# Optimization experiments

Hardware: AMD Instinct MI355X
Metric: run time of the kernel (lower is better)

Reference implementation:

```python
import jax, jax.numpy as jnp
import numpy as np

N, G, E, F, H = 100000, 32768, 1000000, 128, 128

def _mlp(x, w1, b1, w2, b2):
    # Linear -> SiLU -> Linear
    return jax.nn.silu(x @ w1 + b1) @ w2 + b2

def setup_inputs() -> dict:
    key = jax.random.key(0)
    ks = jax.random.split(key, 24)
    s = 0.02
    p = lambda k, shp: (jax.random.normal(k, shp, dtype=jnp.float32) * s)
    inp = {
        "node_features": jax.random.normal(ks[0], (N, F), dtype=jnp.float32),
        "node_pos": jax.random.normal(ks[1], (N, 3), dtype=jnp.float32),
        "grid_pos": jax.random.normal(ks[2], (G, 3), dtype=jnp.float32),
        "edge_index": jax.random.randint(ks[3], (2, E), 0, G, dtype=jnp.int64),
        "orientations": jax.random.normal(ks[4], (N, 3, 3), dtype=jnp.float32),
        # node_model
        "nw1": p(ks[5], (F, H)), "nb1": p(ks[6], (H,)),
        "nw2": p(ks[7], (H, H)), "nb2": p(ks[8], (H,)),
        # edge_model
        "ew1": p(ks[9], (6, H)), "eb1": p(ks[10], (H,)),
        "ew2": p(ks[11], (H, H)), "eb2": p(ks[12], (H,)),
        # message_model
        "mw1": p(ks[13], (2 * H, H)), "mb1": p(ks[14], (H,)),
        "mw2": p(ks[15], (H, H)), "mb2": p(ks[16], (H,)),
        # update_model
        "uw1": p(ks[17], (H, H)), "ub1": p(ks[18], (H,)),
        "uw2": p(ks[19], (H, H)), "ub2": p(ks[20], (H,)),
    }
    return inp

def reference(node_features, node_pos, grid_pos, edge_index, orientations,
              nw1, nb1, nw2, nb2, ew1, eb1, ew2, eb2,
              mw1, mb1, mw2, mb2, uw1, ub1, uw2, ub2):
    src, tgt = edge_index[0], edge_index[1]
    # node MLP on all points [N, H]
    node_h = _mlp(node_features, nw1, nb1, nw2, nb2)
    # per-edge geometry
    pos_src = node_pos[src]                     # [E, 3]
    rel_pos = grid_pos[tgt] - pos_src           # [E, 3]
    # bmm(rel_pos[e,1,3], orientations[src][e,3,3]) -> [E, 3]
    rot = jnp.einsum("ej,ejk->ek", rel_pos, orientations[src])
    edge_attr = jnp.concatenate([pos_src, rot], axis=-1)       # [E, 6]
    edge_h = _mlp(edge_attr, ew1, eb1, ew2, eb2)               # [E, H]
    msg_in = jnp.concatenate([node_h[src], edge_h], axis=-1)   # [E, 2H]
    msg = _mlp(msg_in, mw1, mb1, mw2, mb2)                     # [E, H]
    # scatter-mean to grid
    num_grid = grid_pos.shape[0]
    sums = jax.ops.segment_sum(msg, tgt, num_segments=num_grid)             # [G, H]
    counts = jax.ops.segment_sum(jnp.ones((msg.shape[0],), msg.dtype), tgt,
                                 num_segments=num_grid)
    grid_feat = sums / jnp.clip(counts, 1.0)[:, None]
    return _mlp(grid_feat, uw1, ub1, uw2, ub2)
```

## Files before the change

### kernel.cpp

```cpp
#include <hip/hip_runtime.h>

#define P 136

typedef __attribute__((ext_vector_type(8))) short short8;
typedef __attribute__((ext_vector_type(4))) float f32x4;

__device__ __forceinline__ unsigned short f2bf(float f) {
  union { float f; unsigned u; } v; v.f = f;
  unsigned u = v.u + 0x7fffu + ((v.u >> 16) & 1u);
  return (unsigned short)(u >> 16);
}
__device__ __forceinline__ float bf2f(unsigned short h) {
  union { unsigned u; float f; } v; v.u = ((unsigned)h) << 16;
  return v.f;
}
__device__ __forceinline__ unsigned pack2bf(float x, float y) {
  union { float f; unsigned u; } a, b; a.f = x; b.f = y;
  return __builtin_amdgcn_perm(b.u + 0x8000u, a.u + 0x8000u, 0x07060302u);
}
__device__ __forceinline__ float silu_f(float x) {
  float e = __expf(-x);
  return x * __builtin_amdgcn_rcpf(1.0f + e);
}

__device__ __forceinline__ void load_A128(const unsigned short* __restrict__ W,
                                          int m0w, int l16, int q, short8 a[2][4]) {
#pragma unroll
  for (int rt = 0; rt < 2; ++rt)
#pragma unroll
    for (int kt = 0; kt < 4; ++kt)
      a[rt][kt] = *(const short8*)&W[(m0w + rt * 16 + l16) * 128 + kt * 32 + q * 8];
}

__device__ __forceinline__ void gemm_T(const short8 a[2][4],
                                       const unsigned short* sB,
                                       int l16, int q, f32x4 acc[2][8]) {
#pragma unroll
  for (int kt = 0; kt < 4; ++kt)
#pragma unroll
    for (int ct = 0; ct < 8; ++ct) {
      short8 b = *(const short8*)&sB[(ct * 16 + l16) * P + kt * 32 + q * 8];
      acc[0][ct] = __builtin_amdgcn_mfma_f32_16x16x32_bf16(a[0][kt], b, acc[0][ct], 0, 0, 0);
      acc[1][ct] = __builtin_amdgcn_mfma_f32_16x16x32_bf16(a[1][kt], b, acc[1][ct], 0, 0, 0);
    }
}

template <bool SILU>
__device__ __forceinline__ void epilogue_T(const f32x4 acc[2][8], const float* bias,
                                           unsigned short* sOut, int m0w, int l16,
                                           int q) {
#pragma unroll
  for (int rt = 0; rt < 2; ++rt) {
    int f0 = m0w + rt * 16 + q * 4;
    float4 bv = *(const float4*)&bias[f0];
#pragma unroll
    for (int ct = 0; ct < 8; ++ct) {
      float v0 = acc[rt][ct][0] + bv.x, v1 = acc[rt][ct][1] + bv.y;
      float v2 = acc[rt][ct][2] + bv.z, v3 = acc[rt][ct][3] + bv.w;
      if (SILU) { v0 = silu_f(v0); v1 = silu_f(v1); v2 = silu_f(v2); v3 = silu_f(v3); }
      uint2 w; w.x = pack2bf(v0, v1); w.y = pack2bf(v2, v3);
      *(uint2*)&sOut[(ct * 16 + l16) * P + f0] = w;
    }
  }
}

__global__ __launch_bounds__(256) void fold_hist_kernel(
    const float* __restrict__ nw1, const float* __restrict__ nw2,
    const float* __restrict__ nb2, const float* __restrict__ ew2,
    const float* __restrict__ eb2, const float* __restrict__ mw1,
    const float* __restrict__ mb1, const float* __restrict__ mw2,
    const float* __restrict__ uw1, const float* __restrict__ uw2,
    const float* __restrict__ ew1,
    unsigned short* __restrict__ nw1t, unsigned short* __restrict__ wnt,
    unsigned short* __restrict__ wct, unsigned short* __restrict__ mw2t,
    unsigned short* __restrict__ uw1t, unsigned short* __restrict__ uw2t,
    unsigned short* __restrict__ ew1t8,
    float* __restrict__ bn, float* __restrict__ bc,
    const int* __restrict__ eidx, int* __restrict__ hist, int E) {
  if (blockIdx.x >= 64) {
    int e = (blockIdx.x - 64) * 256 + threadIdx.x;
    if (e < E) atomicAdd(&hist[eidx[E + e]], 1);
    return;
  }
  int b = blockIdx.x * 2 + (threadIdx.x >> 7);
  int t = threadIdx.x & 127;
  float accn = 0.f, accc = 0.f;
  for (int j = 0; j < 128; ++j) {
    accn += nw2[t * 128 + j] * mw1[j * 128 + b];
    accc += ew2[t * 128 + j] * mw1[(128 + j) * 128 + b];
  }
  wnt[b * 128 + t] = f2bf(accn);
  wct[b * 128 + t] = f2bf(accc);
  nw1t[b * 128 + t] = f2bf(nw1[t * 128 + b]);
  mw2t[b * 128 + t] = f2bf(mw2[t * 128 + b]);
  uw1t[b * 128 + t] = f2bf(uw1[t * 128 + b]);
  uw2t[b * 128 + t] = f2bf(uw2[t * 128 + b]);
  if (t < 8) ew1t8[b * 8 + t] = (t < 6) ? f2bf(ew1[t * 128 + b]) : (unsigned short)0;
  if (b == 0) {
    float sn = 0.f, sc = 0.f;
    for (int j = 0; j < 128; ++j) {
      sn += nb2[j] * mw1[j * 128 + t];
      sc += eb2[j] * mw1[(128 + j) * 128 + t];
    }
    bn[t] = sn;
    bc[t] = mb1[t] + sc;
  }
}

__global__ __launch_bounds__(1024) void scan_kernel(const int* __restrict__ hist,
                                                    int* __restrict__ cursor, int G) {
  __shared__ int s[1024];
  int tid = threadIdx.x;
  int per = (G + 1023) >> 10;
  int b0 = tid * per;
  int sum = 0;
  for (int i = 0; i < per; ++i)
    if (b0 + i < G) sum += hist[b0 + i];
  s[tid] = sum;
  __syncthreads();
  for (int off = 1; off < 1024; off <<= 1) {
    int v = (tid >= off) ? s[tid - off] : 0;
    __syncthreads();
    s[tid] += v;
    __syncthreads();
  }
  int run = s[tid] - sum;
  for (int i = 0; i < per; ++i)
    if (b0 + i < G) {
      cursor[b0 + i] = run;
      run += hist[b0 + i];
    }
}

__global__ __launch_bounds__(256, 3) void scatter_node_kernel(
    const int* __restrict__ eidx, int* __restrict__ cursor,
    int2* __restrict__ st, int E, int nScat,
    const float* __restrict__ x, const float* __restrict__ nb1,
    const unsigned short* __restrict__ nw1t, const unsigned short* __restrict__ wnt,
    const float* __restrict__ bn, unsigned short* __restrict__ node_pre, int N) {
  __shared__ __align__(16) unsigned short s_x[128 * P];
  __shared__ __align__(16) float s_b1[128];
  __shared__ __align__(16) float s_bn[128];

  if (blockIdx.x < (unsigned)nScat) {
    int e = blockIdx.x * 256 + threadIdx.x;
    if (e < E) {
      int tg = eidx[E + e];
      int pos = atomicAdd(&cursor[tg], 1);
      st[pos] = make_int2(eidx[e], tg);
    }
    return;
  }

  int tid = threadIdx.x;
  long base = (long)(blockIdx.x - nScat) * 128;

#pragma unroll
  for (int i = 0; i < 16; ++i) {
    int flat = tid + i * 256;
    int row = flat >> 5;
    int c4 = (flat & 31) << 2;
    float4 v = make_float4(0.f, 0.f, 0.f, 0.f);
    if (base + row < N) v = *(const float4*)&x[(base + row) * 128 + c4];
    uint2 w; w.x = pack2bf(v.x, v.y); w.y = pack2bf(v.z, v.w);
    *(uint2*)&s_x[row * P + c4] = w;
  }
  if (tid < 128) { s_b1[tid] = nb1[tid]; s_bn[tid] = bn[tid]; }
  __syncthreads();

  int wave = tid >> 6, lane = tid & 63;
  int q = lane >> 4, l16 = lane & 15;
  int m0w = wave * 32;

  short8 a1[2][4];
  load_A128(nw1t, m0w, l16, q, a1);
  f32x4 acc[2][8];
#pragma unroll
  for (int rt = 0; rt < 2; ++rt)
#pragma unroll
    for (int ct = 0; ct < 8; ++ct) acc[rt][ct] = (f32x4){0.f, 0.f, 0.f, 0.f};
  gemm_T(a1, s_x, l16, q, acc);
  __syncthreads();
  epilogue_T<true>(acc, s_b1, s_x, m0w, l16, q);
  __syncthreads();

  short8 a2[2][4];
  load_A128(wnt, m0w, l16, q, a2);
#pragma unroll
  for (int rt = 0; rt < 2; ++rt)
#pragma unroll
    for (int ct = 0; ct < 8; ++ct) acc[rt][ct] = (f32x4){0.f, 0.f, 0.f, 0.f};
  gemm_T(a2, s_x, l16, q, acc);

#pragma unroll
  for (int rt = 0; rt < 2; ++rt) {
    int f0 = m0w + rt * 16 + q * 4;
    float4 bv = *(const float4*)&s_bn[f0];
#pragma unroll
    for (int ct = 0; ct < 8; ++ct) {
      long n = base + ct * 16 + l16;
      if (n < N) {
        uint2 w;
        w.x = pack2bf(acc[rt][ct][0] + bv.x, acc[rt][ct][1] + bv.y);
        w.y = pack2bf(acc[rt][ct][2] + bv.z, acc[rt][ct][3] + bv.w);
        *(uint2*)&node_pre[n * 128 + f0] = w;
      }
    }
  }
}

__global__ __launch_bounds__(256, 3) void edge_kernel(
    const int2* __restrict__ st_sorted, const float* __restrict__ node_pos,
    const float* __restrict__ grid_pos, const float* __restrict__ ori,
    const unsigned short* __restrict__ ew1t8, const float* __restrict__ eb1,
    const unsigned short* __restrict__ wct, const float* __restrict__ bc,
    const unsigned short* __restrict__ node_pre, float* __restrict__ sums, int E) {
  __shared__ __align__(16) unsigned short s_h[128 * P];
  __shared__ int s_src[128];
  __shared__ int s_tgt[128];
  __shared__ __align__(16) float s_eb1[128];
  __shared__ __align__(16) float s_bc[128];

  int tid = threadIdx.x;
  int base = blockIdx.x * 128;

  if (tid < 128) {
    s_eb1[tid] = eb1[tid];
    s_bc[tid] = bc[tid];
    int eg = base + tid;
    int s = 0, tg = -1;
    float a0 = 0.f, a1 = 0.f, a2 = 0.f, a3 = 0.f, a4 = 0.f, a5 = 0.f;
    if (eg < E) {
      int2 st = st_sorted[eg];
      s = st.x; tg = st.y;
      float2 p01 = *(const float2*)&node_pos[s * 3];
      float pz = node_pos[s * 3 + 2];
      float2 g01 = *(const float2*)&grid_pos[tg * 3];
      float gz = grid_pos[tg * 3 + 2];
      float4 o0 = *(const float4*)&ori[(long)s * 9];
      float4 o1 = *(const float4*)&ori[(long)s * 9 + 4];
      float o8 = ori[(long)s * 9 + 8];
      float rx = g01.x - p01.x, ry = g01.y - p01.y, rz = gz - pz;
      a0 = p01.x; a1 = p01.y; a2 = pz;
      a3 = rx * o0.x + ry * o0.w + rz * o1.z;
      a4 = rx * o0.y + ry * o1.x + rz * o1.w;
      a5 = rx * o0.z + ry * o1.y + rz * o8;
    }
    s_src[tid] = s;
    s_tgt[tid] = tg;
    uint4 w0;
    w0.x = pack2bf(a0, a1); w0.y = pack2bf(a2, a3); w0.z = pack2bf(a4, a5); w0.w = 0u;
    *(uint4*)&s_h[tid * P] = w0;
  }

  int wave = tid >> 6, lane = tid & 63;
  int q = lane >> 4, l16 = lane & 15;
  int m0w = wave * 32;
  short8 z8 = (short8){0, 0, 0, 0, 0, 0, 0, 0};

  short8 ae0 = z8, ae1 = z8;
  if (q == 0) {
    ae0 = *(const short8*)&ew1t8[(m0w + l16) * 8];
    ae1 = *(const short8*)&ew1t8[(m0w + 16 + l16) * 8];
  }

  __syncthreads();

  short8 pre[8];
#pragma unroll
  for (int ct = 0; ct < 8; ++ct) {
    long srow = (long)s_src[ct * 16 + l16] * 128;
    pre[ct] = *(const short8*)&node_pre[srow + m0w + q * 8];
  }

  f32x4 acc0[2][8];
#pragma unroll
  for (int rt = 0; rt < 2; ++rt)
#pragma unroll
    for (int ct = 0; ct < 8; ++ct) acc0[rt][ct] = (f32x4){0.f, 0.f, 0.f, 0.f};
#pragma unroll
  for (int ct = 0; ct < 8; ++ct) {
    short8 b = z8;
    if (q == 0) b = *(const short8*)&s_h[(ct * 16 + l16) * P];
    acc0[0][ct] = __builtin_amdgcn_mfma_f32_16x16x32_bf16(ae0, b, acc0[0][ct], 0, 0, 0);
    acc0[1][ct] = __builtin_amdgcn_mfma_f32_16x16x32_bf16(ae1, b, acc0[1][ct], 0, 0, 0);
  }
  __syncthreads();

  epilogue_T<true>(acc0, s_eb1, s_h, m0w, l16, q);

  short8 awc[2][4];
  load_A128(wct, m0w, l16, q, awc);

  __syncthreads();

  short8 aI_lo, aI_hi;
#pragma unroll
  for (int j = 0; j < 8; ++j) {
    aI_lo[j] = ((q * 8 + j) == l16) ? (short)0x3F80 : (short)0;
    aI_hi[j] = ((q * 8 + j) == (l16 + 16)) ? (short)0x3F80 : (short)0;
  }
  f32x4 acc[2][8];
#pragma unroll
  for (int ct = 0; ct < 8; ++ct) {
    acc[0][ct] = __builtin_amdgcn_mfma_f32_16x16x32_bf16(
        aI_lo, pre[ct], (f32x4){0.f, 0.f, 0.f, 0.f}, 0, 0, 0);
    acc[1][ct] = __builtin_amdgcn_mfma_f32_16x16x32_bf16(
        aI_hi, pre[ct], (f32x4){0.f, 0.f, 0.f, 0.f}, 0, 0, 0);
  }

  gemm_T(awc, s_h, l16, q, acc);
  __syncthreads();

  epilogue_T<true>(acc, s_bc, s_h, m0w, l16, q);
  __syncthreads();

  {
    int cp = tid & 63;
    int chunk = tid >> 6;
    int c0 = cp * 2;
    int row0 = chunk * 32;
    float v0 = 0.f, v1 = 0.f;
    int cur = s_tgt[row0];
    for (int r = 0; r < 32; ++r) {
      int row = row0 + r;
      int tg = s_tgt[row];
      if (tg != cur) {
        if (cur >= 0) {
          atomicAdd(&sums[(long)cur * 128 + c0], v0);
          atomicAdd(&sums[(long)cur * 128 + c0 + 1], v1);
        }
        v0 = 0.f; v1 = 0.f; cur = tg;
      }
      unsigned w = *(const unsigned*)&s_h[row * P + c0];
      v0 += bf2f((unsigned short)w);
      v1 += bf2f((unsigned short)(w >> 16));
    }
    if (cur >= 0) {
      atomicAdd(&sums[(long)cur * 128 + c0], v0);
      atomicAdd(&sums[(long)cur * 128 + c0 + 1], v1);
    }
  }
}

__global__ __launch_bounds__(256, 3) void grid_kernel(
    const float* __restrict__ sums, const int* __restrict__ hist,
    const float* __restrict__ mb2, const float* __restrict__ ub1,
    const float* __restrict__ ub2, const unsigned short* __restrict__ mw2t,
    const unsigned short* __restrict__ uw1t, const unsigned short* __restrict__ uw2t,
    float* __restrict__ out, int G) {
  __shared__ __align__(16) unsigned short s_x[128 * P];
  __shared__ __align__(16) float s_bm[128];
  __shared__ __align__(16) float s_b1[128];
  __shared__ __align__(16) float s_b2[128];
  int tid = threadIdx.x;
  long base = (long)blockIdx.x * 128;

#pragma unroll
  for (int i = 0; i < 16; ++i) {
    int flat = tid + i * 256;
    int row = flat >> 5;
    int c4 = (flat & 31) << 2;
    float4 v = make_float4(0.f, 0.f, 0.f, 0.f);
    float inv = 1.f;
    if (base + row < G) {
      v = *(const float4*)&sums[(base + row) * 128 + c4];
      int c = hist[base + row];
      inv = __builtin_amdgcn_rcpf((float)(c < 1 ? 1 : c));
    }
    uint2 w; w.x = pack2bf(v.x * inv, v.y * inv); w.y = pack2bf(v.z * inv, v.w * inv);
    *(uint2*)&s_x[row * P + c4] = w;
  }
  if (tid < 128) { s_bm[tid] = mb2[tid]; s_b1[tid] = ub1[tid]; s_b2[tid] = ub2[tid]; }
  __syncthreads();

  int wave = tid >> 6, lane = tid & 63;
  int q = lane >> 4, l16 = lane & 15;
  int m0w = wave * 32;

  f32x4 acc[2][8];
  short8 aw[2][4];

  load_A128(mw2t, m0w, l16, q, aw);
#pragma unroll
  for (int rt = 0; rt < 2; ++rt)
#pragma unroll
    for (int ct = 0; ct < 8; ++ct) acc[rt][ct] = (f32x4){0.f, 0.f, 0.f, 0.f};
  gemm_T(aw, s_x, l16, q, acc);
  __syncthreads();
  epilogue_T<false>(acc, s_bm, s_x, m0w, l16, q);
  __syncthreads();

  load_A128(uw1t, m0w, l16, q, aw);
#pragma unroll
  for (int rt = 0; rt < 2; ++rt)
#pragma unroll
    for (int ct = 0; ct < 8; ++ct) acc[rt][ct] = (f32x4){0.f, 0.f, 0.f, 0.f};
  gemm_T(aw, s_x, l16, q, acc);
  __syncthreads();
  epilogue_T<true>(acc, s_b1, s_x, m0w, l16, q);
  __syncthreads();

  load_A128(uw2t, m0w, l16, q, aw);
#pragma unroll
  for (int rt = 0; rt < 2; ++rt)
#pragma unroll
    for (int ct = 0; ct < 8; ++ct) acc[rt][ct] = (f32x4){0.f, 0.f, 0.f, 0.f};
  gemm_T(aw, s_x, l16, q, acc);

#pragma unroll
  for (int rt = 0; rt < 2; ++rt) {
    int f0 = m0w + rt * 16 + q * 4;
    float4 bv = *(const float4*)&s_b2[f0];
#pragma unroll
    for (int ct = 0; ct < 8; ++ct) {
      long g = base + ct * 16 + l16;
      if (g < G) {
        float4 o = make_float4(acc[rt][ct][0] + bv.x, acc[rt][ct][1] + bv.y,
                               acc[rt][ct][2] + bv.z, acc[rt][ct][3] + bv.w);
        *(float4*)&out[g * 128 + f0] = o;
      }
    }
  }
}

extern "C" void kernel_launch(void* const* d_in, const int* in_sizes, int n_in,
                              void* d_out, int out_size, void* d_ws, size_t ws_size,
                              hipStream_t stream) {
  const float* x    = (const float*)d_in[0];
  const float* npos = (const float*)d_in[1];
  const float* gpos = (const float*)d_in[2];
  const int*   eidx = (const int*)d_in[3];
  const float* ori  = (const float*)d_in[4];
  const float* nw1 = (const float*)d_in[5];
  const float* nb1 = (const float*)d_in[6];
  const float* nw2 = (const float*)d_in[7];
  const float* nb2 = (const float*)d_in[8];
  const float* ew1 = (const float*)d_in[9];
  const float* eb1 = (const float*)d_in[10];
  const float* ew2 = (const float*)d_in[11];
  const float* eb2 = (const float*)d_in[12];
  const float* mw1 = (const float*)d_in[13];
  const float* mb1 = (const float*)d_in[14];
  const float* mw2 = (const float*)d_in[15];
  const float* mb2 = (const float*)d_in[16];
  const float* uw1 = (const float*)d_in[17];
  const float* ub1 = (const float*)d_in[18];
  const float* uw2 = (const float*)d_in[19];
  const float* ub2 = (const float*)d_in[20];

  int N = in_sizes[0] / 128;
  int G = in_sizes[2] / 3;
  int E = in_sizes[3] / 2;

  char* ws = (char*)d_ws;
  size_t off = 0;
  float* sums = (float*)(ws + off);            off += (size_t)G * 128 * 4;
  int* hist = (int*)(ws + off);                off += (size_t)G * 4;
  int* cursor = (int*)(ws + off);              off += (size_t)G * 4;
  unsigned short* node_pre = (unsigned short*)(ws + off); off += (size_t)N * 128 * 2;
  off = (off + 255) & ~(size_t)255;
  unsigned short* w_nw1t = (unsigned short*)(ws + off); off += 128 * 128 * 2;
  unsigned short* w_wnt  = (unsigned short*)(ws + off); off += 128 * 128 * 2;
  unsigned short* w_wct  = (unsigned short*)(ws + off); off += 128 * 128 * 2;
  unsigned short* w_mw2t = (unsigned short*)(ws + off); off += 128 * 128 * 2;
  unsigned short* w_uw1t = (unsigned short*)(ws + off); off += 128 * 128 * 2;
  unsigned short* w_uw2t = (unsigned short*)(ws + off); off += 128 * 128 * 2;
  unsigned short* w_ew1t8 = (unsigned short*)(ws + off); off += 128 * 8 * 2;
  float* bn = (float*)(ws + off); off += 128 * 4;
  float* bc = (float*)(ws + off); off += 128 * 4;

  int2* st_sorted = (int2*)d_out;

  int nScat = (E + 255) / 256;
  int nNode = (N + 127) / 128;
  int nHist = (E + 255) / 256;

  hipMemsetAsync(sums, 0, ((size_t)G * 128 + G) * 4, stream);

  fold_hist_kernel<<<64 + nHist, 256, 0, stream>>>(
      nw1, nw2, nb2, ew2, eb2, mw1, mb1, mw2, uw1, uw2, ew1,
      w_nw1t, w_wnt, w_wct, w_mw2t, w_uw1t, w_uw2t, w_ew1t8, bn, bc,
      eidx, hist, E);
  scan_kernel<<<1, 1024, 0, stream>>>(hist, cursor, G);
  scatter_node_kernel<<<nScat + nNode, 256, 0, stream>>>(
      eidx, cursor, st_sorted, E, nScat,
      x, nb1, w_nw1t, w_wnt, bn, node_pre, N);
  edge_kernel<<<(E + 127) / 128, 256, 0, stream>>>(st_sorted, npos, gpos, ori,
                                                   w_ew1t8, eb1, w_wct, bc,
                                                   node_pre, sums, E);
  grid_kernel<<<(G + 127) / 128, 256, 0, stream>>>(sums, hist, mb2, ub1, ub2,
                                                   w_mw2t, w_uw1t, w_uw2t,
                                                   (float*)d_out, G);
}
```

Baseline: 469.3 us.

## Batch eight edges per thread in hist/scatter, shrink grid tiles, templatize GEMM

The histogram and scatter phases now handle eight edges per thread using int4 loads, which cuts the number of blocks launched. The scan kernel reads and writes counts with int4 where alignment allows. The grid kernel tile drops from 128 to 32 grid points per block, giving four times as many smaller blocks with less shared memory each, which should help occupancy and load balance. The GEMM helper is templated on the column-tile count and seeds the first MFMA with zero instead of clearing accumulators in a separate loop, and the scatter blocks are moved after the node blocks. The trade-off is that smaller grid tiles reload the weights more often, and batching edges leaves fewer threads in flight to hide atomic latency.

```diff
diff --git a/kernel.cpp b/kernel.cpp
--- a/kernel.cpp
+++ b/kernel.cpp
@@ -32,21 +32,25 @@
       a[rt][kt] = *(const short8*)&W[(m0w + rt * 16 + l16) * 128 + kt * 32 + q * 8];
 }
 
+template <int CT, bool INIT>
 __device__ __forceinline__ void gemm_T(const short8 a[2][4],
                                        const unsigned short* sB,
-                                       int l16, int q, f32x4 acc[2][8]) {
+                                       int l16, int q, f32x4 acc[2][CT]) {
+  const f32x4 Z = (f32x4){0.f, 0.f, 0.f, 0.f};
 #pragma unroll
   for (int kt = 0; kt < 4; ++kt)
 #pragma unroll
-    for (int ct = 0; ct < 8; ++ct) {
+    for (int ct = 0; ct < CT; ++ct) {
       short8 b = *(const short8*)&sB[(ct * 16 + l16) * P + kt * 32 + q * 8];
-      acc[0][ct] = __builtin_amdgcn_mfma_f32_16x16x32_bf16(a[0][kt], b, acc[0][ct], 0, 0, 0);
-      acc[1][ct] = __builtin_amdgcn_mfma_f32_16x16x32_bf16(a[1][kt], b, acc[1][ct], 0, 0, 0);
-    }
-}
-
-template <bool SILU>
-__device__ __forceinline__ void epilogue_T(const f32x4 acc[2][8], const float* bias,
+      f32x4 c0 = (INIT && kt == 0) ? Z : acc[0][ct];
+      f32x4 c1 = (INIT && kt == 0) ? Z : acc[1][ct];
+      acc[0][ct] = __builtin_amdgcn_mfma_f32_16x16x32_bf16(a[0][kt], b, c0, 0, 0, 0);
+      acc[1][ct] = __builtin_amdgcn_mfma_f32_16x16x32_bf16(a[1][kt], b, c1, 0, 0, 0);
+    }
+}
+
+template <bool SILU, int CT>
+__device__ __forceinline__ void epilogue_T(const f32x4 acc[2][CT], const float* bias,
                                            unsigned short* sOut, int m0w, int l16,
                                            int q) {
 #pragma unroll
@@ -54,7 +58,7 @@
     int f0 = m0w + rt * 16 + q * 4;
     float4 bv = *(const float4*)&bias[f0];
 #pragma unroll
-    for (int ct = 0; ct < 8; ++ct) {
+    for (int ct = 0; ct < CT; ++ct) {
       float v0 = acc[rt][ct][0] + bv.x, v1 = acc[rt][ct][1] + bv.y;
       float v2 = acc[rt][ct][2] + bv.z, v3 = acc[rt][ct][3] + bv.w;
       if (SILU) { v0 = silu_f(v0); v1 = silu_f(v1); v2 = silu_f(v2); v3 = silu_f(v3); }
@@ -78,8 +82,21 @@
     float* __restrict__ bn, float* __restrict__ bc,
     const int* __restrict__ eidx, int* __restrict__ hist, int E) {
   if (blockIdx.x >= 64) {
-    int e = (blockIdx.x - 64) * 256 + threadIdx.x;
-    if (e < E) atomicAdd(&hist[eidx[E + e]], 1);
+    int e0 = (blockIdx.x - 64) * 2048 + threadIdx.x * 8;
+    if (e0 + 7 < E && (E & 3) == 0) {
+      int4 t0 = *(const int4*)&eidx[E + e0];
+      int4 t1 = *(const int4*)&eidx[E + e0 + 4];
+      atomicAdd(&hist[t0.x], 1); atomicAdd(&hist[t0.y], 1);
+      atomicAdd(&hist[t0.z], 1); atomicAdd(&hist[t0.w], 1);
+      atomicAdd(&hist[t1.x], 1); atomicAdd(&hist[t1.y], 1);
+      atomicAdd(&hist[t1.z], 1); atomicAdd(&hist[t1.w], 1);
+    } else {
+#pragma unroll
+      for (int k = 0; k < 8; ++k) {
+        int e = e0 + k;
+        if (e < E) atomicAdd(&hist[eidx[E + e]], 1);
+      }
+    }
     return;
   }
   int b = blockIdx.x * 2 + (threadIdx.x >> 7);
@@ -113,9 +130,17 @@
   int tid = threadIdx.x;
   int per = (G + 1023) >> 10;
   int b0 = tid * per;
+  bool vec = ((per & 3) == 0) && ((G & 3) == 0) && (b0 + per <= G);
   int sum = 0;
-  for (int i = 0; i < per; ++i)
-    if (b0 + i < G) sum += hist[b0 + i];
+  if (vec) {
+    for (int i = 0; i < per; i += 4) {
+      int4 h = *(const int4*)&hist[b0 + i];
+      sum += h.x + h.y + h.z + h.w;
+    }
+  } else {
+    for (int i = 0; i < per; ++i)
+      if (b0 + i < G) sum += hist[b0 + i];
+  }
   s[tid] = sum;
   __syncthreads();
   for (int off = 1; off < 1024; off <<= 1) {
@@ -125,16 +150,29 @@
     __syncthreads();
   }
   int run = s[tid] - sum;
-  for (int i = 0; i < per; ++i)
-    if (b0 + i < G) {
-      cursor[b0 + i] = run;
-      run += hist[b0 + i];
-    }
+  if (vec) {
+    for (int i = 0; i < per; i += 4) {
+      int4 h = *(const int4*)&hist[b0 + i];
+      int4 c;
+      c.x = run;
+      c.y = c.x + h.x;
+      c.z = c.y + h.y;
+      c.w = c.z + h.z;
+      *(int4*)&cursor[b0 + i] = c;
+      run = c.w + h.w;
+    }
+  } else {
+    for (int i = 0; i < per; ++i)
+      if (b0 + i < G) {
+        cursor[b0 + i] = run;
+        run += hist[b0 + i];
+      }
+  }
 }
 
 __global__ __launch_bounds__(256, 3) void scatter_node_kernel(
     const int* __restrict__ eidx, int* __restrict__ cursor,
-    int2* __restrict__ st, int E, int nScat,
+    int2* __restrict__ st, int E, int nNode,
     const float* __restrict__ x, const float* __restrict__ nb1,
     const unsigned short* __restrict__ nw1t, const unsigned short* __restrict__ wnt,
     const float* __restrict__ bn, unsigned short* __restrict__ node_pre, int N) {
@@ -142,18 +180,45 @@
   __shared__ __align__(16) float s_b1[128];
   __shared__ __align__(16) float s_bn[128];
 
-  if (blockIdx.x < (unsigned)nScat) {
-    int e = blockIdx.x * 256 + threadIdx.x;
-    if (e < E) {
-      int tg = eidx[E + e];
-      int pos = atomicAdd(&cursor[tg], 1);
-      st[pos] = make_int2(eidx[e], tg);
+  if (blockIdx.x >= (unsigned)nNode) {
+    int e0 = (blockIdx.x - nNode) * 2048 + threadIdx.x * 8;
+    if (e0 + 7 < E && (E & 3) == 0) {
+      int4 s0 = *(const int4*)&eidx[e0];
+      int4 s1 = *(const int4*)&eidx[e0 + 4];
+      int4 t0 = *(const int4*)&eidx[E + e0];
+      int4 t1 = *(const int4*)&eidx[E + e0 + 4];
+      int p0 = atomicAdd(&cursor[t0.x], 1);
+      int p1 = atomicAdd(&cursor[t0.y], 1);
+      int p2 = atomicAdd(&cursor[t0.z], 1);
+      int p3 = atomicAdd(&cursor[t0.w], 1);
+      int p4 = atomicAdd(&cursor[t1.x], 1);
+      int p5 = atomicAdd(&cursor[t1.y], 1);
+      int p6 = atomicAdd(&cursor[t1.z], 1);
+      int p7 = atomicAdd(&cursor[t1.w], 1);
+      st[p0] = make_int2(s0.x, t0.x);
+      st[p1] = make_int2(s0.y, t0.y);
+      st[p2] = make_int2(s0.z, t0.z);
+      st[p3] = make_int2(s0.w, t0.w);
+      st[p4] = make_int2(s1.x, t1.x);
+      st[p5] = make_int2(s1.y, t1.y);
+      st[p6] = make_int2(s1.z, t1.z);
+      st[p7] = make_int2(s1.w, t1.w);
+    } else {
+#pragma unroll
+      for (int k = 0; k < 8; ++k) {
+        int e = e0 + k;
+        if (e < E) {
+          int tg = eidx[E + e];
+          int pos = atomicAdd(&cursor[tg], 1);
+          st[pos] = make_int2(eidx[e], tg);
+        }
+      }
     }
     return;
   }
 
   int tid = threadIdx.x;
-  long base = (long)(blockIdx.x - nScat) * 128;
+  long base = (long)blockIdx.x * 128;
 
 #pragma unroll
   for (int i = 0; i < 16; ++i) {
@@ -175,22 +240,14 @@
   short8 a1[2][4];
   load_A128(nw1t, m0w, l16, q, a1);
   f32x4 acc[2][8];
-#pragma unroll
-  for (int rt = 0; rt < 2; ++rt)
-#pragma unroll
-    for (int ct = 0; ct < 8; ++ct) acc[rt][ct] = (f32x4){0.f, 0.f, 0.f, 0.f};
-  gemm_T(a1, s_x, l16, q, acc);
-  __syncthreads();
-  epilogue_T<true>(acc, s_b1, s_x, m0w, l16, q);
+  gemm_T<8, true>(a1, s_x, l16, q, acc);
+  __syncthreads();
+  epilogue_T<true, 8>(acc, s_b1, s_x, m0w, l16, q);
   __syncthreads();
 
   short8 a2[2][4];
   load_A128(wnt, m0w, l16, q, a2);
-#pragma unroll
-  for (int rt = 0; rt < 2; ++rt)
-#pragma unroll
-    for (int ct = 0; ct < 8; ++ct) acc[rt][ct] = (f32x4){0.f, 0.f, 0.f, 0.f};
-  gemm_T(a2, s_x, l16, q, acc);
+  gemm_T<8, true>(a2, s_x, l16, q, acc);
 
 #pragma unroll
   for (int rt = 0; rt < 2; ++rt) {
@@ -257,6 +314,7 @@
   int q = lane >> 4, l16 = lane & 15;
   int m0w = wave * 32;
   short8 z8 = (short8){0, 0, 0, 0, 0, 0, 0, 0};
+  const f32x4 Z = (f32x4){0.f, 0.f, 0.f, 0.f};
 
   short8 ae0 = z8, ae1 = z8;
   if (q == 0) {
@@ -273,21 +331,17 @@
     pre[ct] = *(const short8*)&node_pre[srow + m0w + q * 8];
   }
 
-  f32x4 acc0[2][8];
-#pragma unroll
-  for (int rt = 0; rt < 2; ++rt)
-#pragma unroll
-    for (int ct = 0; ct < 8; ++ct) acc0[rt][ct] = (f32x4){0.f, 0.f, 0.f, 0.f};
+  f32x4 acc[2][8];
 #pragma unroll
   for (int ct = 0; ct < 8; ++ct) {
     short8 b = z8;
     if (q == 0) b = *(const short8*)&s_h[(ct * 16 + l16) * P];
-    acc0[0][ct] = __builtin_amdgcn_mfma_f32_16x16x32_bf16(ae0, b, acc0[0][ct], 0, 0, 0);
-    acc0[1][ct] = __builtin_amdgcn_mfma_f32_16x16x32_bf16(ae1, b, acc0[1][ct], 0, 0, 0);
-  }
-  __syncthreads();
-
-  epilogue_T<true>(acc0, s_eb1, s_h, m0w, l16, q);
+    acc[0][ct] = __builtin_amdgcn_mfma_f32_16x16x32_bf16(ae0, b, Z, 0, 0, 0);
+    acc[1][ct] = __builtin_amdgcn_mfma_f32_16x16x32_bf16(ae1, b, Z, 0, 0, 0);
+  }
+  __syncthreads();
+
+  epilogue_T<true, 8>(acc, s_eb1, s_h, m0w, l16, q);
 
   short8 awc[2][4];
   load_A128(wct, m0w, l16, q, awc);
@@ -300,19 +354,16 @@
     aI_lo[j] = ((q * 8 + j) == l16) ? (short)0x3F80 : (short)0;
     aI_hi[j] = ((q * 8 + j) == (l16 + 16)) ? (short)0x3F80 : (short)0;
   }
-  f32x4 acc[2][8];
 #pragma unroll
   for (int ct = 0; ct < 8; ++ct) {
-    acc[0][ct] = __builtin_amdgcn_mfma_f32_16x16x32_bf16(
-        aI_lo, pre[ct], (f32x4){0.f, 0.f, 0.f, 0.f}, 0, 0, 0);
-    acc[1][ct] = __builtin_amdgcn_mfma_f32_16x16x32_bf16(
-        aI_hi, pre[ct], (f32x4){0.f, 0.f, 0.f, 0.f}, 0, 0, 0);
-  }
-
-  gemm_T(awc, s_h, l16, q, acc);
-  __syncthreads();
-
-  epilogue_T<true>(acc, s_bc, s_h, m0w, l16, q);
+    acc[0][ct] = __builtin_amdgcn_mfma_f32_16x16x32_bf16(aI_lo, pre[ct], Z, 0, 0, 0);
+    acc[1][ct] = __builtin_amdgcn_mfma_f32_16x16x32_bf16(aI_hi, pre[ct], Z, 0, 0, 0);
+  }
+
+  gemm_T<8, false>(awc, s_h, l16, q, acc);
+  __syncthreads();
+
+  epilogue_T<true, 8>(acc, s_bc, s_h, m0w, l16, q);
   __syncthreads();
 
   {
@@ -349,15 +400,15 @@
     const float* __restrict__ ub2, const unsigned short* __restrict__ mw2t,
     const unsigned short* __restrict__ uw1t, const unsigned short* __restrict__ uw2t,
     float* __restrict__ out, int G) {
-  __shared__ __align__(16) unsigned short s_x[128 * P];
+  __shared__ __align__(16) unsigned short s_x[32 * P];
   __shared__ __align__(16) float s_bm[128];
   __shared__ __align__(16) float s_b1[128];
   __shared__ __align__(16) float s_b2[128];
   int tid = threadIdx.x;
-  long base = (long)blockIdx.x * 128;
-
-#pragma unroll
-  for (int i = 0; i < 16; ++i) {
+  long base = (long)blockIdx.x * 32;
+
+#pragma unroll
+  for (int i = 0; i < 4; ++i) {
     int flat = tid + i * 256;
     int row = flat >> 5;
     int c4 = (flat & 31) << 2;
@@ -378,42 +429,30 @@
   int q = lane >> 4, l16 = lane & 15;
   int m0w = wave * 32;
 
-  f32x4 acc[2][8];
+  f32x4 acc[2][2];
   short8 aw[2][4];
 
   load_A128(mw2t, m0w, l16, q, aw);
-#pragma unroll
-  for (int rt = 0; rt < 2; ++rt)
-#pragma unroll
-    for (int ct = 0; ct < 8; ++ct) acc[rt][ct] = (f32x4){0.f, 0.f, 0.f, 0.f};
-  gemm_T(aw, s_x, l16, q, acc);
-  __syncthreads();
-  epilogue_T<false>(acc, s_bm, s_x, m0w, l16, q);
+  gemm_T<2, true>(aw, s_x, l16, q, acc);
+  __syncthreads();
+  epilogue_T<false, 2>(acc, s_bm, s_x, m0w, l16, q);
   __syncthreads();
 
   load_A128(uw1t, m0w, l16, q, aw);
-#pragma unroll
-  for (int rt = 0; rt < 2; ++rt)
-#pragma unroll
-    for (int ct = 0; ct < 8; ++ct) acc[rt][ct] = (f32x4){0.f, 0.f, 0.f, 0.f};
-  gemm_T(aw, s_x, l16, q, acc);
-  __syncthreads();
-  epilogue_T<true>(acc, s_b1, s_x, m0w, l16, q);
+  gemm_T<2, true>(aw, s_x, l16, q, acc);
+  __syncthreads();
+  epilogue_T<true, 2>(acc, s_b1, s_x, m0w, l16, q);
   __syncthreads();
 
   load_A128(uw2t, m0w, l16, q, aw);
-#pragma unroll
-  for (int rt = 0; rt < 2; ++rt)
-#pragma unroll
-    for (int ct = 0; ct < 8; ++ct) acc[rt][ct] = (f32x4){0.f, 0.f, 0.f, 0.f};
-  gemm_T(aw, s_x, l16, q, acc);
+  gemm_T<2, true>(aw, s_x, l16, q, acc);
 
 #pragma unroll
   for (int rt = 0; rt < 2; ++rt) {
     int f0 = m0w + rt * 16 + q * 4;
     float4 bv = *(const float4*)&s_b2[f0];
 #pragma unroll
-    for (int ct = 0; ct < 8; ++ct) {
+    for (int ct = 0; ct < 2; ++ct) {
       long g = base + ct * 16 + l16;
       if (g < G) {
         float4 o = make_float4(acc[rt][ct][0] + bv.x, acc[rt][ct][1] + bv.y,
@@ -472,9 +511,9 @@
 
   int2* st_sorted = (int2*)d_out;
 
-  int nScat = (E + 255) / 256;
+  int nScat = (E + 2047) / 2048;
   int nNode = (N + 127) / 128;
-  int nHist = (E + 255) / 256;
+  int nHist = (E + 2047) / 2048;
 
   hipMemsetAsync(sums, 0, ((size_t)G * 128 + G) * 4, stream);
 
@@ -483,13 +522,13 @@
       w_nw1t, w_wnt, w_wct, w_mw2t, w_uw1t, w_uw2t, w_ew1t8, bn, bc,
       eidx, hist, E);
   scan_kernel<<<1, 1024, 0, stream>>>(hist, cursor, G);
-  scatter_node_kernel<<<nScat + nNode, 256, 0, stream>>>(
-      eidx, cursor, st_sorted, E, nScat,
+  scatter_node_kernel<<<nNode + nScat, 256, 0, stream>>>(
+      eidx, cursor, st_sorted, E, nNode,
       x, nb1, w_nw1t, w_wnt, bn, node_pre, N);
   edge_kernel<<<(E + 127) / 128, 256, 0, stream>>>(st_sorted, npos, gpos, ori,
                                                    w_ew1t8, eb1, w_wct, bc,
                                                    node_pre, sums, E);
-  grid_kernel<<<(G + 127) / 128, 256, 0, stream>>>(sums, hist, mb2, ub1, ub2,
-                                                   w_mw2t, w_uw1t, w_uw2t,
-                                                   (float*)d_out, G);
-}
+  grid_kernel<<<(G + 31) / 32, 256, 0, stream>>>(sums, hist, mb2, ub1, ub2,
+                                                 w_mw2t, w_uw1t, w_uw2t,
+                                                 (float*)d_out, G);
+}
```

After: 395.9 us. 15.6% less time.
